# Kernel optimization log

Hardware: AMD Instinct MI355X
Metric: run time of the kernel (lower is better)

## Reference

```python
import jax, jax.numpy as jnp
import numpy as np

N_SRC = 100000
N_DST = 100000
E = 1250000
IN_SRC = 64
IN_DST = 64
OUT = 64


def setup_inputs() -> dict:
    key = jax.random.key(0)
    k = jax.random.split(key, 7)
    x_src = jax.random.normal(k[0], (N_SRC, IN_SRC), dtype=jnp.float32)
    x_dst = jax.random.normal(k[1], (N_DST, IN_DST), dtype=jnp.float32)
    edge_index_sd = jax.random.randint(k[2], (2, E), 0, N_SRC, dtype=jnp.int64)
    edge_weight = jax.random.uniform(k[3], (E,), dtype=jnp.float32)
    # Linear params (torch: y = x @ W.T + b), kaiming-ish scale
    W_nei = jax.random.normal(k[4], (OUT, IN_SRC), dtype=jnp.float32) / np.sqrt(IN_SRC)
    W_self = jax.random.normal(k[5], (OUT, IN_DST), dtype=jnp.float32) / np.sqrt(IN_DST)
    b_self = jax.random.normal(k[6], (OUT,), dtype=jnp.float32) / np.sqrt(IN_DST)
    return {"x_src": x_src, "x_dst": x_dst, "edge_index_sd": edge_index_sd,
            "edge_weight": edge_weight, "W_nei": W_nei, "W_self": W_self,
            "b_self": b_self}


def reference(x_src, x_dst, edge_index_sd, edge_weight, W_nei, W_self, b_self):
    src_idx = edge_index_sd[0]
    dst_idx = edge_index_sd[1]
    # self term: [N_dst, out]
    out = x_dst @ W_self.T + b_self
    # neighbor transform then gather per edge: [E, out]
    h_src = x_src @ W_nei.T
    msg = h_src[src_idx] * edge_weight[:, None]
    # scatter-add into dst rows
    out = out.at[dst_idx].add(msg)
    return out
```

## Files before the change

### kernel.cpp

```cpp
#include <hip/hip_runtime.h>

#define NN 100000
#define FD 64
#define NE 1250000

#define RPB 128
#define NBK ((NN + RPB - 1) / RPB)
#define NBP 1024
#define CAP 2048
#define CH  8192
#define NCH ((NE + CH - 1) / CH)
#define NTILE (NN / 16)

#define TPW 2
#define NWM (NTILE / TPW)
#define LIN_GRID ((2 * NWM + 3) / 4)

typedef __attribute__((ext_vector_type(8))) short bf16x8;
typedef __attribute__((ext_vector_type(4))) float f32x4;

__device__ __forceinline__ short cvt_bf16(float f) {
    unsigned u = __float_as_uint(f);
    return (short)((u + 0x7FFFu + ((u >> 16) & 1u)) >> 16);
}
__device__ __forceinline__ float bf2f(unsigned short u) {
    return __uint_as_float(((unsigned)u) << 16);
}

__global__ __launch_bounds__(256) void lin_both(
    const float* __restrict__ x_src, const float* __restrict__ x_dst,
    const float* __restrict__ W_nei, const float* __restrict__ W_self,
    const float* __restrict__ b_self, unsigned short* __restrict__ hbuf,
    float* __restrict__ out, int* __restrict__ gcur)
{
    if (gcur && blockIdx.x == 0) {
        #pragma unroll
        for (int i = 0; i < NBP / 256; i++) gcur[threadIdx.x + i * 256] = 0;
    }
    const int lane = threadIdx.x & 63;
    const int m    = lane & 15;
    const int quad = lane >> 4;
    const int gw   = blockIdx.x * 4 + (threadIdx.x >> 6);
    if (gw >= 2 * NWM) return;
    const bool self = gw >= NWM;
    const int  wm   = self ? gw - NWM : gw;
    const float* __restrict__ x = self ? x_dst : x_src;
    const float* __restrict__ W = self ? W_self : W_nei;

    const float* xb = x + (size_t)(wm * (TPW * 16) + m) * FD;
    float4 xv[TPW][4];
    #pragma unroll
    for (int t = 0; t < TPW; t++) {
        const float* xr = xb + (size_t)t * 16 * FD;
        xv[t][0] = *(const float4*)(xr + quad * 8);
        xv[t][1] = *(const float4*)(xr + quad * 8 + 4);
        xv[t][2] = *(const float4*)(xr + 32 + quad * 8);
        xv[t][3] = *(const float4*)(xr + 32 + quad * 8 + 4);
    }

    bf16x8 wf[2][4];
    #pragma unroll
    for (int kc = 0; kc < 2; kc++) {
        #pragma unroll
        for (int ct = 0; ct < 4; ct++) {
            const float4 w0 = *(const float4*)(W + (ct * 16 + m) * FD + kc * 32 + quad * 8);
            const float4 w1 = *(const float4*)(W + (ct * 16 + m) * FD + kc * 32 + quad * 8 + 4);
            bf16x8 f;
            f[0]=cvt_bf16(w0.x); f[1]=cvt_bf16(w0.y); f[2]=cvt_bf16(w0.z); f[3]=cvt_bf16(w0.w);
            f[4]=cvt_bf16(w1.x); f[5]=cvt_bf16(w1.y); f[6]=cvt_bf16(w1.z); f[7]=cvt_bf16(w1.w);
            wf[kc][ct] = f;
        }
    }

    float4 bv[4];
    if (self) {
        #pragma unroll
        for (int ct = 0; ct < 4; ct++)
            bv[ct] = *(const float4*)(b_self + ct * 16 + quad * 4);
    }

    #pragma unroll
    for (int t = 0; t < TPW; t++) {
        bf16x8 a0, a1;
        a0[0]=cvt_bf16(xv[t][0].x); a0[1]=cvt_bf16(xv[t][0].y);
        a0[2]=cvt_bf16(xv[t][0].z); a0[3]=cvt_bf16(xv[t][0].w);
        a0[4]=cvt_bf16(xv[t][1].x); a0[5]=cvt_bf16(xv[t][1].y);
        a0[6]=cvt_bf16(xv[t][1].z); a0[7]=cvt_bf16(xv[t][1].w);
        a1[0]=cvt_bf16(xv[t][2].x); a1[1]=cvt_bf16(xv[t][2].y);
        a1[2]=cvt_bf16(xv[t][2].z); a1[3]=cvt_bf16(xv[t][2].w);
        a1[4]=cvt_bf16(xv[t][3].x); a1[5]=cvt_bf16(xv[t][3].y);
        a1[6]=cvt_bf16(xv[t][3].z); a1[7]=cvt_bf16(xv[t][3].w);

        f32x4 acc[4];
        #pragma unroll
        for (int ct = 0; ct < 4; ct++) {
            f32x4 z = (f32x4){0.f, 0.f, 0.f, 0.f};
            z = __builtin_amdgcn_mfma_f32_16x16x32_bf16(wf[0][ct], a0, z, 0, 0, 0);
            z = __builtin_amdgcn_mfma_f32_16x16x32_bf16(wf[1][ct], a1, z, 0, 0, 0);
            acc[ct] = z;
        }

        const size_t rowbase = (size_t)(wm * (TPW * 16) + t * 16 + m) * FD;
        if (!self) {
            #pragma unroll
            for (int ct = 0; ct < 4; ct++) {
                ushort4 sv;
                sv.x = (unsigned short)cvt_bf16(acc[ct][0]);
                sv.y = (unsigned short)cvt_bf16(acc[ct][1]);
                sv.z = (unsigned short)cvt_bf16(acc[ct][2]);
                sv.w = (unsigned short)cvt_bf16(acc[ct][3]);
                *(ushort4*)(hbuf + rowbase + ct * 16 + quad * 4) = sv;
            }
        } else {
            #pragma unroll
            for (int ct = 0; ct < 4; ct++) {
                float4 v;
                v.x = acc[ct][0] + bv[ct].x;
                v.y = acc[ct][1] + bv[ct].y;
                v.z = acc[ct][2] + bv[ct].z;
                v.w = acc[ct][3] + bv[ct].w;
                *(float4*)(out + rowbase + ct * 16 + quad * 4) = v;
            }
        }
    }
}

__global__ __launch_bounds__(1024) void kplace(
    const int* __restrict__ src, const int* __restrict__ dst,
    const float* __restrict__ ew, int* __restrict__ gcursor,
    int2* __restrict__ sp)
{
    __shared__ int cnt[NBP];
    const int t = threadIdx.x;
    if (t < NBP) cnt[t] = 0;
    __syncthreads();
    const int e0 = blockIdx.x * CH;

    int d[8];
    #pragma unroll
    for (int k = 0; k < 8; k++) {
        const int e = e0 + t + k * 1024;
        d[k] = (e < NE) ? dst[e] : -1;
    }
    #pragma unroll
    for (int k = 0; k < 8; k++)
        if (d[k] >= 0) atomicAdd(&cnt[d[k] >> 7], 1);
    __syncthreads();

    if (t < NBP) {
        const int c = cnt[t];
        cnt[t] = c ? (t * CAP + atomicAdd(&gcursor[t], c)) : 0;
    }
    __syncthreads();

    int s[8]; float w[8];
    #pragma unroll
    for (int k = 0; k < 8; k++) {
        const int e = e0 + t + k * 1024;
        if (e < NE) { s[k] = src[e]; w[k] = ew[e]; }
    }
    #pragma unroll
    for (int k = 0; k < 8; k++) {
        if (d[k] >= 0) {
            const int p = atomicAdd(&cnt[d[k] >> 7], 1);
            sp[p] = make_int2(s[k] | ((d[k] & (RPB - 1)) << 17),
                              __float_as_int(w[k]));
        }
    }
}

__global__ __launch_bounds__(512) void sort_gather(
    const int2* __restrict__ sp, const int* __restrict__ gcursor,
    const unsigned short* __restrict__ h, float* __restrict__ out)
{
    __shared__ int2 ebuf[CAP + 16];
    __shared__ int hist[RPB];
    __shared__ int rs[RPB];
    __shared__ int cur[RPB];
    const int t = threadIdx.x;
    const int b = blockIdx.x;
    const int cnt = gcursor[b];
    const int s0 = b * CAP;

    if (t < RPB) hist[t] = 0;

    int2 ev[4]; int er[4];
    #pragma unroll
    for (int k = 0; k < 4; k++) {
        const int j = t + k * 512;
        if (j < cnt) { ev[k] = sp[s0 + j]; er[k] = ev[k].x >> 17; }
        else er[k] = -1;
    }
    __syncthreads();
    #pragma unroll
    for (int k = 0; k < 4; k++)
        if (er[k] >= 0) atomicAdd(&hist[er[k]], 1);
    __syncthreads();
    if (t < 64) {
        const int v0 = hist[2*t], v1 = hist[2*t + 1];
        const int s = v0 + v1;
        int inc = s;
        #pragma unroll
        for (int off = 1; off < 64; off <<= 1) {
            int u = __shfl_up(inc, off, 64);
            if (t >= off) inc += u;
        }
        const int ex = inc - s;
        rs[2*t]      = ex;       cur[2*t]     = ex;
        rs[2*t + 1]  = ex + v0;  cur[2*t + 1] = ex + v0;
    }
    __syncthreads();
    #pragma unroll
    for (int k = 0; k < 4; k++) {
        if (er[k] >= 0) {
            const int p = atomicAdd(&cur[er[k]], 1);
            ebuf[p] = ev[k];
        }
    }
    if (t < 16) ebuf[cnt + t] = make_int2(0, 0);
    __syncthreads();

    const int wv   = t >> 6;
    const int lane = t & 63;
    const int q    = lane >> 4;
    const int tc   = lane & 15;
    const unsigned tb = (unsigned)tc << 3;
    const int row0 = b * RPB;

    #pragma unroll
    for (int i = 0; i < 4; i++) {
        const int r   = i * 32 + wv * 4 + q;
        const int row = row0 + r;
        if (row >= NN) continue;
        const int rsr = rs[r];
        const int n   = hist[r];
        float a0 = 0.f, a1 = 0.f, a2 = 0.f, a3 = 0.f;
        for (int k = 0; k < n; k += 4) {
            int2 ed[4];
            #pragma unroll
            for (int j = 0; j < 4; j++)
                ed[j] = ebuf[rsr + k + j];
            uint2 dv[4]; float wv4[4];
            #pragma unroll
            for (int j = 0; j < 4; j++) {
                const unsigned off = (((unsigned)(ed[j].x & 0x1FFFF)) << 7) | tb;
                dv[j] = *(const uint2*)((const char*)h + off);
                wv4[j] = (k + j < n) ? __int_as_float(ed[j].y) : 0.f;
            }
            #pragma unroll
            for (int j = 0; j < 4; j++) {
                const float w = wv4[j];
                a0 = fmaf(__uint_as_float(dv[j].x << 16),         w, a0);
                a1 = fmaf(__uint_as_float(dv[j].x & 0xFFFF0000u), w, a1);
                a2 = fmaf(__uint_as_float(dv[j].y << 16),         w, a2);
                a3 = fmaf(__uint_as_float(dv[j].y & 0xFFFF0000u), w, a3);
            }
        }
        float4* p = (float4*)(out + (size_t)row * FD + (tc << 2));
        float4 v = *p;
        v.x += a0; v.y += a1; v.z += a2; v.w += a3;
        *p = v;
    }
}

__global__ __launch_bounds__(256) void scatter_edges(
    const unsigned short* __restrict__ h, const int* __restrict__ eidx,
    const float* __restrict__ ew, float* __restrict__ out)
{
    const int lane  = threadIdx.x & 63;
    const int gwave = (int)((blockIdx.x * blockDim.x + threadIdx.x) >> 6);
    const int nwave = (int)((gridDim.x * blockDim.x) >> 6);
    const int* __restrict__ src = eidx;
    const int* __restrict__ dst = eidx + NE;
    for (int e = gwave; e < NE; e += nwave) {
        const float v = bf2f(h[(size_t)src[e] * FD + lane]) * ew[e];
        atomicAdd(out + (size_t)dst[e] * FD + lane, v);
    }
}

extern "C" void kernel_launch(void* const* d_in, const int* in_sizes, int n_in,
                              void* d_out, int out_size, void* d_ws, size_t ws_size,
                              hipStream_t stream)
{
    const float* x_src  = (const float*)d_in[0];
    const float* x_dst  = (const float*)d_in[1];
    const int*   eidx   = (const int*)  d_in[2];
    const float* ew     = (const float*)d_in[3];
    const float* W_nei  = (const float*)d_in[4];
    const float* W_self = (const float*)d_in[5];
    const float* b_self = (const float*)d_in[6];
    float* out = (float*)d_out;

    const int* src = eidx;
    const int* dst = eidx + NE;

    char* ws = (char*)d_ws;
    size_t off = 0;
    auto alloc = [&](size_t bytes) { char* p = ws + off; off += (bytes + 15) & ~(size_t)15; return p; };
    unsigned short* h = (unsigned short*)alloc((size_t)NN * FD * sizeof(unsigned short));
    int*  gcursor  = (int*) alloc((size_t)NBP * sizeof(int));
    int2* sp       = (int2*)alloc((size_t)NBP * CAP * sizeof(int2));
    const size_t need_main = off;
    const size_t need_h    = (size_t)NN * FD * sizeof(unsigned short);

    if (ws_size >= need_main) {
        lin_both<<<LIN_GRID, 256, 0, stream>>>(x_src, x_dst, W_nei, W_self,
                                               b_self, h, out, gcursor);
        kplace<<<NCH, 1024, 0, stream>>>(src, dst, ew, gcursor, sp);
        sort_gather<<<NBK, 512, 0, stream>>>(sp, gcursor, h, out);
    } else if (ws_size >= need_h) {
        lin_both<<<LIN_GRID, 256, 0, stream>>>(x_src, x_dst, W_nei, W_self,
                                               b_self, h, out, nullptr);
        scatter_edges<<<2048, 256, 0, stream>>>(h, eidx, ew, out);
    }
}
```

Measured before the change: 171.4 us.

## Fuse self linear transform into sort_gather epilogue

After: 172.1 us. Within noise of the previous version (+0.4%).

```diff
diff --git a/kernel.cpp b/kernel.cpp
--- a/kernel.cpp
+++ b/kernel.cpp
@@ -15,6 +15,9 @@
 #define TPW 2
 #define NWM (NTILE / TPW)
 #define LIN_GRID ((2 * NWM + 3) / 4)
+#define NEI_GRID ((NWM + 3) / 4)
+
+#define SLP 68
 
 typedef __attribute__((ext_vector_type(8))) short bf16x8;
 typedef __attribute__((ext_vector_type(4))) float f32x4;
@@ -25,18 +28,242 @@
 }
 __device__ __forceinline__ float bf2f(unsigned short u) {
     return __uint_as_float(((unsigned)u) << 16);
+}
+__device__ __forceinline__ bf16x8 cvt8(const float4& a, const float4& b) {
+    bf16x8 f;
+    f[0]=cvt_bf16(a.x); f[1]=cvt_bf16(a.y); f[2]=cvt_bf16(a.z); f[3]=cvt_bf16(a.w);
+    f[4]=cvt_bf16(b.x); f[5]=cvt_bf16(b.y); f[6]=cvt_bf16(b.z); f[7]=cvt_bf16(b.w);
+    return f;
+}
+
+__global__ __launch_bounds__(256) void lin_nei(
+    const float* __restrict__ x_src, const float* __restrict__ W_nei,
+    unsigned short* __restrict__ hbuf, int* __restrict__ gcur)
+{
+    if (blockIdx.x == 0) {
+        #pragma unroll
+        for (int i = 0; i < NBP / 256; i++) gcur[threadIdx.x + i * 256] = 0;
+    }
+    const int lane = threadIdx.x & 63;
+    const int m    = lane & 15;
+    const int quad = lane >> 4;
+    const int gw   = blockIdx.x * 4 + (threadIdx.x >> 6);
+    if (gw >= NWM) return;
+
+    const float* xb = x_src + (size_t)(gw * (TPW * 16) + m) * FD;
+    float4 xv[TPW][4];
+    #pragma unroll
+    for (int t = 0; t < TPW; t++) {
+        const float* xr = xb + (size_t)t * 16 * FD;
+        xv[t][0] = *(const float4*)(xr + quad * 8);
+        xv[t][1] = *(const float4*)(xr + quad * 8 + 4);
+        xv[t][2] = *(const float4*)(xr + 32 + quad * 8);
+        xv[t][3] = *(const float4*)(xr + 32 + quad * 8 + 4);
+    }
+    bf16x8 wf[2][4];
+    #pragma unroll
+    for (int kc = 0; kc < 2; kc++) {
+        #pragma unroll
+        for (int ct = 0; ct < 4; ct++) {
+            const float4 w0 = *(const float4*)(W_nei + (ct * 16 + m) * FD + kc * 32 + quad * 8);
+            const float4 w1 = *(const float4*)(W_nei + (ct * 16 + m) * FD + kc * 32 + quad * 8 + 4);
+            wf[kc][ct] = cvt8(w0, w1);
+        }
+    }
+    #pragma unroll
+    for (int t = 0; t < TPW; t++) {
+        const bf16x8 a0 = cvt8(xv[t][0], xv[t][1]);
+        const bf16x8 a1 = cvt8(xv[t][2], xv[t][3]);
+        const size_t rowbase = (size_t)(gw * (TPW * 16) + t * 16 + m) * FD;
+        #pragma unroll
+        for (int ct = 0; ct < 4; ct++) {
+            f32x4 z = (f32x4){0.f, 0.f, 0.f, 0.f};
+            z = __builtin_amdgcn_mfma_f32_16x16x32_bf16(wf[0][ct], a0, z, 0, 0, 0);
+            z = __builtin_amdgcn_mfma_f32_16x16x32_bf16(wf[1][ct], a1, z, 0, 0, 0);
+            ushort4 sv;
+            sv.x = (unsigned short)cvt_bf16(z[0]);
+            sv.y = (unsigned short)cvt_bf16(z[1]);
+            sv.z = (unsigned short)cvt_bf16(z[2]);
+            sv.w = (unsigned short)cvt_bf16(z[3]);
+            *(ushort4*)(hbuf + rowbase + ct * 16 + quad * 4) = sv;
+        }
+    }
+}
+
+__global__ __launch_bounds__(1024) void kplace(
+    const int* __restrict__ src, const int* __restrict__ dst,
+    const float* __restrict__ ew, int* __restrict__ gcursor,
+    int2* __restrict__ sp)
+{
+    __shared__ int cnt[NBP];
+    const int t = threadIdx.x;
+    if (t < NBP) cnt[t] = 0;
+    __syncthreads();
+    const int e0 = blockIdx.x * CH;
+
+    int d[8];
+    #pragma unroll
+    for (int k = 0; k < 8; k++) {
+        const int e = e0 + t + k * 1024;
+        d[k] = (e < NE) ? dst[e] : -1;
+    }
+    #pragma unroll
+    for (int k = 0; k < 8; k++)
+        if (d[k] >= 0) atomicAdd(&cnt[d[k] >> 7], 1);
+    __syncthreads();
+
+    if (t < NBP) {
+        const int c = cnt[t];
+        cnt[t] = c ? (t * CAP + atomicAdd(&gcursor[t], c)) : 0;
+    }
+    __syncthreads();
+
+    int s[8]; float w[8];
+    #pragma unroll
+    for (int k = 0; k < 8; k++) {
+        const int e = e0 + t + k * 1024;
+        if (e < NE) { s[k] = src[e]; w[k] = ew[e]; }
+    }
+    #pragma unroll
+    for (int k = 0; k < 8; k++) {
+        if (d[k] >= 0) {
+            const int p = atomicAdd(&cnt[d[k] >> 7], 1);
+            sp[p] = make_int2(s[k] | ((d[k] & (RPB - 1)) << 17),
+                              __float_as_int(w[k]));
+        }
+    }
+}
+
+__global__ __launch_bounds__(512) void sort_gather(
+    const int2* __restrict__ sp, const int* __restrict__ gcursor,
+    const unsigned short* __restrict__ h, const float* __restrict__ x_dst,
+    const float* __restrict__ W_self, const float* __restrict__ b_self,
+    float* __restrict__ out)
+{
+    __shared__ int2 ebuf[CAP + 16];
+    __shared__ int hist[RPB];
+    __shared__ int rs[RPB];
+    __shared__ int cur[RPB];
+    __shared__ float self_lds[RPB * SLP];
+    const int t = threadIdx.x;
+    const int b = blockIdx.x;
+    const int cnt = gcursor[b];
+    const int s0 = b * CAP;
+    const int row0 = b * RPB;
+    const int wv   = t >> 6;
+    const int lane = t & 63;
+    const int m    = lane & 15;
+    const int quad = lane >> 4;
+
+    int xrow = row0 + wv * 16 + m;
+    if (xrow >= NN) xrow = NN - 1;
+    const float* xr = x_dst + (size_t)xrow * FD;
+    const float4 x0 = *(const float4*)(xr + quad * 8);
+    const float4 x1 = *(const float4*)(xr + quad * 8 + 4);
+    const float4 x2 = *(const float4*)(xr + 32 + quad * 8);
+    const float4 x3 = *(const float4*)(xr + 32 + quad * 8 + 4);
+
+    if (t < RPB) hist[t] = 0;
+
+    int2 ev[4]; int er[4];
+    #pragma unroll
+    for (int k = 0; k < 4; k++) {
+        const int j = t + k * 512;
+        if (j < cnt) { ev[k] = sp[s0 + j]; er[k] = ev[k].x >> 17; }
+        else er[k] = -1;
+    }
+    __syncthreads();
+    #pragma unroll
+    for (int k = 0; k < 4; k++)
+        if (er[k] >= 0) atomicAdd(&hist[er[k]], 1);
+    __syncthreads();
+    if (t < 64) {
+        const int v0 = hist[2*t], v1 = hist[2*t + 1];
+        const int s = v0 + v1;
+        int inc = s;
+        #pragma unroll
+        for (int off = 1; off < 64; off <<= 1) {
+            int u = __shfl_up(inc, off, 64);
+            if (t >= off) inc += u;
+        }
+        const int ex = inc - s;
+        rs[2*t]      = ex;       cur[2*t]     = ex;
+        rs[2*t + 1]  = ex + v0;  cur[2*t + 1] = ex + v0;
+    }
+    __syncthreads();
+    #pragma unroll
+    for (int k = 0; k < 4; k++) {
+        if (er[k] >= 0) {
+            const int p = atomicAdd(&cur[er[k]], 1);
+            ebuf[p] = ev[k];
+        }
+    }
+    if (t < 16) ebuf[cnt + t] = make_int2(0, 0);
+
+    {
+        const bf16x8 a0 = cvt8(x0, x1);
+        const bf16x8 a1 = cvt8(x2, x3);
+        #pragma unroll
+        for (int ct = 0; ct < 4; ct++) {
+            const float4 w0 = *(const float4*)(W_self + (ct * 16 + m) * FD + quad * 8);
+            const float4 w1 = *(const float4*)(W_self + (ct * 16 + m) * FD + quad * 8 + 4);
+            const float4 w2 = *(const float4*)(W_self + (ct * 16 + m) * FD + 32 + quad * 8);
+            const float4 w3 = *(const float4*)(W_self + (ct * 16 + m) * FD + 32 + quad * 8 + 4);
+            f32x4 z = (f32x4){0.f, 0.f, 0.f, 0.f};
+            z = __builtin_amdgcn_mfma_f32_16x16x32_bf16(cvt8(w0, w1), a0, z, 0, 0, 0);
+            z = __builtin_amdgcn_mfma_f32_16x16x32_bf16(cvt8(w2, w3), a1, z, 0, 0, 0);
+            const float4 bb = *(const float4*)(b_self + ct * 16 + quad * 4);
+            float4 v;
+            v.x = z[0] + bb.x; v.y = z[1] + bb.y;
+            v.z = z[2] + bb.z; v.w = z[3] + bb.w;
+            *(float4*)&self_lds[(wv * 16 + m) * SLP + ct * 16 + quad * 4] = v;
+        }
+    }
+    __syncthreads();
+
+    const unsigned tb = (unsigned)m << 3;
+    #pragma unroll
+    for (int i = 0; i < 4; i++) {
+        const int r   = i * 32 + wv * 4 + quad;
+        const int row = row0 + r;
+        if (row >= NN) continue;
+        const int rsr = rs[r];
+        const int n   = hist[r];
+        float a0 = 0.f, a1 = 0.f, a2 = 0.f, a3 = 0.f;
+        for (int k = 0; k < n; k += 4) {
+            int2 ed[4];
+            #pragma unroll
+            for (int j = 0; j < 4; j++)
+                ed[j] = ebuf[rsr + k + j];
+            uint2 dv[4]; float wv4[4];
+            #pragma unroll
+            for (int j = 0; j < 4; j++) {
+                const unsigned off = (((unsigned)(ed[j].x & 0x1FFFF)) << 7) | tb;
+                dv[j] = *(const uint2*)((const char*)h + off);
+                wv4[j] = (k + j < n) ? __int_as_float(ed[j].y) : 0.f;
+            }
+            #pragma unroll
+            for (int j = 0; j < 4; j++) {
+                const float w = wv4[j];
+                a0 = fmaf(__uint_as_float(dv[j].x << 16),         w, a0);
+                a1 = fmaf(__uint_as_float(dv[j].x & 0xFFFF0000u), w, a1);
+                a2 = fmaf(__uint_as_float(dv[j].y << 16),         w, a2);
+                a3 = fmaf(__uint_as_float(dv[j].y & 0xFFFF0000u), w, a3);
+            }
+        }
+        const float4 sv = *(const float4*)&self_lds[r * SLP + (m << 2)];
+        float4 v;
+        v.x = sv.x + a0; v.y = sv.y + a1; v.z = sv.z + a2; v.w = sv.w + a3;
+        *(float4*)(out + (size_t)row * FD + (m << 2)) = v;
+    }
 }
 
 __global__ __launch_bounds__(256) void lin_both(
     const float* __restrict__ x_src, const float* __restrict__ x_dst,
     const float* __restrict__ W_nei, const float* __restrict__ W_self,
     const float* __restrict__ b_self, unsigned short* __restrict__ hbuf,
-    float* __restrict__ out, int* __restrict__ gcur)
-{
-    if (gcur && blockIdx.x == 0) {
-        #pragma unroll
-        for (int i = 0; i < NBP / 256; i++) gcur[threadIdx.x + i * 256] = 0;
-    }
+    float* __restrict__ out)
+{
     const int lane = threadIdx.x & 63;
     const int m    = lane & 15;
     const int quad = lane >> 4;
@@ -57,7 +284,6 @@
         xv[t][2] = *(const float4*)(xr + 32 + quad * 8);
         xv[t][3] = *(const float4*)(xr + 32 + quad * 8 + 4);
     }
-
     bf16x8 wf[2][4];
     #pragma unroll
     for (int kc = 0; kc < 2; kc++) {
@@ -65,32 +291,19 @@
         for (int ct = 0; ct < 4; ct++) {
             const float4 w0 = *(const float4*)(W + (ct * 16 + m) * FD + kc * 32 + quad * 8);
             const float4 w1 = *(const float4*)(W + (ct * 16 + m) * FD + kc * 32 + quad * 8 + 4);
-            bf16x8 f;
-            f[0]=cvt_bf16(w0.x); f[1]=cvt_bf16(w0.y); f[2]=cvt_bf16(w0.z); f[3]=cvt_bf16(w0.w);
-            f[4]=cvt_bf16(w1.x); f[5]=cvt_bf16(w1.y); f[6]=cvt_bf16(w1.z); f[7]=cvt_bf16(w1.w);
-            wf[kc][ct] = f;
-        }
-    }
-
+            wf[kc][ct] = cvt8(w0, w1);
+        }
+    }
     float4 bv[4];
     if (self) {
         #pragma unroll
         for (int ct = 0; ct < 4; ct++)
             bv[ct] = *(const float4*)(b_self + ct * 16 + quad * 4);
     }
-
     #pragma unroll
     for (int t = 0; t < TPW; t++) {
-        bf16x8 a0, a1;
-        a0[0]=cvt_bf16(xv[t][0].x); a0[1]=cvt_bf16(xv[t][0].y);
-        a0[2]=cvt_bf16(xv[t][0].z); a0[3]=cvt_bf16(xv[t][0].w);
-        a0[4]=cvt_bf16(xv[t][1].x); a0[5]=cvt_bf16(xv[t][1].y);
-        a0[6]=cvt_bf16(xv[t][1].z); a0[7]=cvt_bf16(xv[t][1].w);
-        a1[0]=cvt_bf16(xv[t][2].x); a1[1]=cvt_bf16(xv[t][2].y);
-        a1[2]=cvt_bf16(xv[t][2].z); a1[3]=cvt_bf16(xv[t][2].w);
-        a1[4]=cvt_bf16(xv[t][3].x); a1[5]=cvt_bf16(xv[t][3].y);
-        a1[6]=cvt_bf16(xv[t][3].z); a1[7]=cvt_bf16(xv[t][3].w);
-
+        const bf16x8 a0 = cvt8(xv[t][0], xv[t][1]);
+        const bf16x8 a1 = cvt8(xv[t][2], xv[t][3]);
         f32x4 acc[4];
         #pragma unroll
         for (int ct = 0; ct < 4; ct++) {
@@ -99,7 +312,6 @@
             z = __builtin_amdgcn_mfma_f32_16x16x32_bf16(wf[1][ct], a1, z, 0, 0, 0);
             acc[ct] = z;
         }
-
         const size_t rowbase = (size_t)(wm * (TPW * 16) + t * 16 + m) * FD;
         if (!self) {
             #pragma unroll
@@ -125,144 +337,6 @@
     }
 }
 
-__global__ __launch_bounds__(1024) void kplace(
-    const int* __restrict__ src, const int* __restrict__ dst,
-    const float* __restrict__ ew, int* __restrict__ gcursor,
-    int2* __restrict__ sp)
-{
-    __shared__ int cnt[NBP];
-    const int t = threadIdx.x;
-    if (t < NBP) cnt[t] = 0;
-    __syncthreads();
-    const int e0 = blockIdx.x * CH;
-
-    int d[8];
-    #pragma unroll
-    for (int k = 0; k < 8; k++) {
-        const int e = e0 + t + k * 1024;
-        d[k] = (e < NE) ? dst[e] : -1;
-    }
-    #pragma unroll
-    for (int k = 0; k < 8; k++)
-        if (d[k] >= 0) atomicAdd(&cnt[d[k] >> 7], 1);
-    __syncthreads();
-
-    if (t < NBP) {
-        const int c = cnt[t];
-        cnt[t] = c ? (t * CAP + atomicAdd(&gcursor[t], c)) : 0;
-    }
-    __syncthreads();
-
-    int s[8]; float w[8];
-    #pragma unroll
-    for (int k = 0; k < 8; k++) {
-        const int e = e0 + t + k * 1024;
-        if (e < NE) { s[k] = src[e]; w[k] = ew[e]; }
-    }
-    #pragma unroll
-    for (int k = 0; k < 8; k++) {
-        if (d[k] >= 0) {
-            const int p = atomicAdd(&cnt[d[k] >> 7], 1);
-            sp[p] = make_int2(s[k] | ((d[k] & (RPB - 1)) << 17),
-                              __float_as_int(w[k]));
-        }
-    }
-}
-
-__global__ __launch_bounds__(512) void sort_gather(
-    const int2* __restrict__ sp, const int* __restrict__ gcursor,
-    const unsigned short* __restrict__ h, float* __restrict__ out)
-{
-    __shared__ int2 ebuf[CAP + 16];
-    __shared__ int hist[RPB];
-    __shared__ int rs[RPB];
-    __shared__ int cur[RPB];
-    const int t = threadIdx.x;
-    const int b = blockIdx.x;
-    const int cnt = gcursor[b];
-    const int s0 = b * CAP;
-
-    if (t < RPB) hist[t] = 0;
-
-    int2 ev[4]; int er[4];
-    #pragma unroll
-    for (int k = 0; k < 4; k++) {
-        const int j = t + k * 512;
-        if (j < cnt) { ev[k] = sp[s0 + j]; er[k] = ev[k].x >> 17; }
-        else er[k] = -1;
-    }
-    __syncthreads();
-    #pragma unroll
-    for (int k = 0; k < 4; k++)
-        if (er[k] >= 0) atomicAdd(&hist[er[k]], 1);
-    __syncthreads();
-    if (t < 64) {
-        const int v0 = hist[2*t], v1 = hist[2*t + 1];
-        const int s = v0 + v1;
-        int inc = s;
-        #pragma unroll
-        for (int off = 1; off < 64; off <<= 1) {
-            int u = __shfl_up(inc, off, 64);
-            if (t >= off) inc += u;
-        }
-        const int ex = inc - s;
-        rs[2*t]      = ex;       cur[2*t]     = ex;
-        rs[2*t + 1]  = ex + v0;  cur[2*t + 1] = ex + v0;
-    }
-    __syncthreads();
-    #pragma unroll
-    for (int k = 0; k < 4; k++) {
-        if (er[k] >= 0) {
-            const int p = atomicAdd(&cur[er[k]], 1);
-            ebuf[p] = ev[k];
-        }
-    }
-    if (t < 16) ebuf[cnt + t] = make_int2(0, 0);
-    __syncthreads();
-
-    const int wv   = t >> 6;
-    const int lane = t & 63;
-    const int q    = lane >> 4;
-    const int tc   = lane & 15;
-    const unsigned tb = (unsigned)tc << 3;
-    const int row0 = b * RPB;
-
-    #pragma unroll
-    for (int i = 0; i < 4; i++) {
-        const int r   = i * 32 + wv * 4 + q;
-        const int row = row0 + r;
-        if (row >= NN) continue;
-        const int rsr = rs[r];
-        const int n   = hist[r];
-        float a0 = 0.f, a1 = 0.f, a2 = 0.f, a3 = 0.f;
-        for (int k = 0; k < n; k += 4) {
-            int2 ed[4];
-            #pragma unroll
-            for (int j = 0; j < 4; j++)
-                ed[j] = ebuf[rsr + k + j];
-            uint2 dv[4]; float wv4[4];
-            #pragma unroll
-            for (int j = 0; j < 4; j++) {
-                const unsigned off = (((unsigned)(ed[j].x & 0x1FFFF)) << 7) | tb;
-                dv[j] = *(const uint2*)((const char*)h + off);
-                wv4[j] = (k + j < n) ? __int_as_float(ed[j].y) : 0.f;
-            }
-            #pragma unroll
-            for (int j = 0; j < 4; j++) {
-                const float w = wv4[j];
-                a0 = fmaf(__uint_as_float(dv[j].x << 16),         w, a0);
-                a1 = fmaf(__uint_as_float(dv[j].x & 0xFFFF0000u), w, a1);
-                a2 = fmaf(__uint_as_float(dv[j].y << 16),         w, a2);
-                a3 = fmaf(__uint_as_float(dv[j].y & 0xFFFF0000u), w, a3);
-            }
-        }
-        float4* p = (float4*)(out + (size_t)row * FD + (tc << 2));
-        float4 v = *p;
-        v.x += a0; v.y += a1; v.z += a2; v.w += a3;
-        *p = v;
-    }
-}
-
 __global__ __launch_bounds__(256) void scatter_edges(
     const unsigned short* __restrict__ h, const int* __restrict__ eidx,
     const float* __restrict__ ew, float* __restrict__ out)
@@ -304,13 +378,13 @@
     const size_t need_h    = (size_t)NN * FD * sizeof(unsigned short);
 
     if (ws_size >= need_main) {
-        lin_both<<<LIN_GRID, 256, 0, stream>>>(x_src, x_dst, W_nei, W_self,
-                                               b_self, h, out, gcursor);
+        lin_nei<<<NEI_GRID, 256, 0, stream>>>(x_src, W_nei, h, gcursor);
         kplace<<<NCH, 1024, 0, stream>>>(src, dst, ew, gcursor, sp);
-        sort_gather<<<NBK, 512, 0, stream>>>(sp, gcursor, h, out);
+        sort_gather<<<NBK, 512, 0, stream>>>(sp, gcursor, h, x_dst,
+                                             W_self, b_self, out);
     } else if (ws_size >= need_h) {
         lin_both<<<LIN_GRID, 256, 0, stream>>>(x_src, x_dst, W_nei, W_self,
-                                               b_self, h, out, nullptr);
+                                               b_self, h, out);
         scatter_edges<<<2048, 256, 0, stream>>>(h, eidx, ew, out);
     }
 }
```
